# Performance work log

Hardware: AMD Instinct MI355X
Metric: run time of the kernel (lower is better)

Reference implementation:

```python
import jax, jax.numpy as jnp
import numpy as np

N, D, H, K, L, C = 65536, 512, 256, 16, 3, 64  # n_support, embed_dim, D//2, max_clusters, num_levels, n_classes
EPS = 1e-5


def setup_inputs() -> dict:
    key = jax.random.key(0)
    ks = jax.random.split(key, 18)
    s = 0.02
    inp = {
        "support_features": jax.random.normal(ks[0], (N, D), jnp.float32),
        "support_labels": jax.random.randint(ks[1], (N,), 0, C),
        # cluster heads (per level): Linear(D,H) -> ReLU -> Linear(H,K) -> Softmax
        "ch_w1": jax.random.normal(ks[2], (L, D, H), jnp.float32) * s,
        "ch_b1": jnp.zeros((L, H), jnp.float32),
        "ch_w2": jax.random.normal(ks[3], (L, H, K), jnp.float32) * s,
        "ch_b2": jnp.zeros((L, K), jnp.float32),
        # prototype refiners (per level): Linear(D,D) -> LayerNorm -> ReLU -> Linear(D,D)
        "ref_w1": jax.random.normal(ks[4], (L, D, D), jnp.float32) * s,
        "ref_b1": jnp.zeros((L, D), jnp.float32),
        "ln_g": jnp.ones((L, D), jnp.float32),
        "ln_b": jnp.zeros((L, D), jnp.float32),
        "ref_w2": jax.random.normal(ks[5], (L, D, D), jnp.float32) * s,
        "ref_b2": jnp.zeros((L, D), jnp.float32),
        # hierarchy combiner: Linear(L*D, D) -> ReLU -> Linear(D, D)
        "comb_w1": jax.random.normal(ks[6], (L * D, D), jnp.float32) * s,
        "comb_b1": jnp.zeros((D,), jnp.float32),
        "comb_w2": jax.random.normal(ks[7], (D, D), jnp.float32) * s,
        "comb_b2": jnp.zeros((D,), jnp.float32),
    }
    return inp


def _layernorm(x, g, b):
    m = x.mean(-1, keepdims=True)
    v = ((x - m) ** 2).mean(-1, keepdims=True)
    return (x - m) * jax.lax.rsqrt(v + EPS) * g + b


def reference(support_features, support_labels, ch_w1, ch_b1, ch_w2, ch_b2,
              ref_w1, ref_b1, ln_g, ln_b, ref_w2, ref_b2,
              comb_w1, comb_b1, comb_w2, comb_b2):
    current = support_features  # [N, D]; per-class offsets applied via label gather
    level_protos = []
    for l in range(L):
        # cluster head; softmax omitted since argmax is softmax-invariant
        logits = jax.nn.relu(current @ ch_w1[l] + ch_b1[l]) @ ch_w2[l] + ch_b2[l]  # [N, K]
        assign = jnp.argmax(logits, axis=-1)  # [N]
        seg = support_labels * K + assign  # combined (class, cluster) segment id
        sums = jax.ops.segment_sum(current, seg, num_segments=C * K)  # [C*K, D]
        cnt = jax.ops.segment_sum(jnp.ones((N,), current.dtype), seg, num_segments=C * K)
        means = sums / jnp.maximum(cnt, 1.0)[:, None]  # empty clusters -> 0, masked below
        h = means @ ref_w1[l] + ref_b1[l]
        h = jax.nn.relu(_layernorm(h, ln_g[l], ln_b[l]))
        refined = (h @ ref_w2[l] + ref_b2[l]).reshape(C, K, D)
        ne = (cnt.reshape(C, K) > 0).astype(current.dtype)  # non-empty cluster mask
        lp = (refined * ne[..., None]).sum(1) / ne.sum(1)[:, None]  # [C, D] mean over non-empty
        level_protos.append(lp)
        current = current + lp[support_labels]
    combined = jnp.concatenate(level_protos, axis=-1)  # [C, L*D]
    protos = jax.nn.relu(combined @ comb_w1 + comb_b1) @ comb_w2 + comb_b2  # [C, D]
    return protos
```

## Files before the change

kernel.cpp:

```cpp
#include <hip/hip_runtime.h>

#define NPTS 65536
#define DIM  512
#define HID  256
#define KCL  16
#define NLVL 3
#define NCLS 64
#define NSEG (NCLS*KCL)
#define EPSF 1e-5f

typedef __bf16 bf16_t;
typedef bf16_t bf16x4 __attribute__((ext_vector_type(4)));
typedef bf16_t bf16x8 __attribute__((ext_vector_type(8)));
typedef float  f32x4  __attribute__((ext_vector_type(4)));

#define LDA 40
#define LDH2 68

__global__ __launch_bounds__(256) void wsplit_kernel(
    const float* __restrict__ w1, bf16_t* __restrict__ hiT, bf16_t* __restrict__ loT)
{
  int gid = blockIdx.x * 256 + threadIdx.x;
  int n = gid >> 9, k = gid & 511;
  int l = n >> 8, j = n & 255;
  float v = w1[l*DIM*HID + k*HID + j];
  bf16_t h = (bf16_t)v;
  hiT[gid] = h;
  loT[gid] = (bf16_t)(v - (float)h);
}

__global__ __launch_bounds__(256) void wsplit2_kernel(
    const float* __restrict__ w1, const float* __restrict__ w2,
    bf16_t* __restrict__ h1, bf16_t* __restrict__ l1,
    bf16_t* __restrict__ h2, bf16_t* __restrict__ l2)
{
  const int per = NLVL*DIM*DIM;
  int gid = blockIdx.x * 256 + threadIdx.x;
  const float* w = (gid < per) ? w1 : w2;
  bf16_t* hh = (gid < per) ? h1 : h2;
  bf16_t* ll = (gid < per) ? l1 : l2;
  int g2 = (gid < per) ? gid : gid - per;
  int n512 = g2 >> 9, k = g2 & 511;
  int l = n512 >> 9, n = n512 & 511;
  float v = w[(size_t)l*DIM*DIM + (size_t)k*DIM + n];
  bf16_t h = (bf16_t)v;
  hh[g2] = h;
  ll[g2] = (bf16_t)(v - (float)h);
}

__global__ __launch_bounds__(256) void wsplitW2_kernel(
    const float* __restrict__ w2, bf16_t* __restrict__ hiT, bf16_t* __restrict__ loT)
{
  int gid = blockIdx.x * 256 + threadIdx.x;
  int l = gid >> 12, rem = gid & 4095;
  int k2 = rem >> 8, k = rem & 255;
  float v = w2[(size_t)l*HID*KCL + k*KCL + k2];
  bf16_t h = (bf16_t)v;
  hiT[gid] = h;
  loT[gid] = (bf16_t)(v - (float)h);
}

__global__ __launch_bounds__(512, 4) void gemmassign_kernel(
    const float* __restrict__ feat,
    const bf16_t* __restrict__ BhiT, const bf16_t* __restrict__ BloT,
    const bf16_t* __restrict__ w2hT, const bf16_t* __restrict__ w2lT,
    const float* __restrict__ offsrc, int ldo,
    const int* __restrict__ labels,
    const float* __restrict__ pb2,
    int* __restrict__ asg, int* __restrict__ cnt)
{
  __shared__ __align__(16) unsigned char SMraw[2*128*LDH2*4];
  __shared__ int labs[128];
  bf16_t* SM  = (bf16_t*)SMraw;
  bf16_t* Ahi = SM;
  bf16_t* Alo = SM + 128*LDA;
  bf16_t* Bhi = SM + 256*LDA;
  bf16_t* Blo = SM + 512*LDA;

  const int t = threadIdx.x;
  const int row0 = blockIdx.x * 128;
  const int w = t >> 6, lane = t & 63;
  const int wm = w & 1, wn = w >> 1;
  const int fm = lane & 15, fq = lane >> 4;

  if (t < 128) labs[t] = labels[row0 + t];
  const float pv = pb2[fm];

  f32x4 acc[4][4];
  #pragma unroll
  for (int i = 0; i < 4; i++)
    #pragma unroll
    for (int j = 0; j < 4; j++)
      #pragma unroll
      for (int r = 0; r < 4; r++) acc[i][j][r] = 0.f;

  for (int kc = 0; kc < DIM; kc += 32) {
    __syncthreads();
    #pragma unroll
    for (int p = 0; p < 2; p++) {
      int idx = t + 512*p;
      int r = idx >> 3, c = idx & 7;
      float4 v = *(const float4*)&feat[(size_t)(row0 + r)*DIM + kc + c*4];
      bf16x4 hi, lo;
      hi[0] = (bf16_t)v.x; lo[0] = (bf16_t)(v.x - (float)hi[0]);
      hi[1] = (bf16_t)v.y; lo[1] = (bf16_t)(v.y - (float)hi[1]);
      hi[2] = (bf16_t)v.z; lo[2] = (bf16_t)(v.z - (float)hi[2]);
      hi[3] = (bf16_t)v.w; lo[3] = (bf16_t)(v.w - (float)hi[3]);
      *(bf16x4*)&Ahi[r*LDA + c*4] = hi;
      *(bf16x4*)&Alo[r*LDA + c*4] = lo;
    }
    #pragma unroll
    for (int p = 0; p < 2; p++) {
      int idx = t + 512*p;
      int n = idx >> 2, c = idx & 3;
      *(bf16x8*)&Bhi[n*LDA + c*8] = *(const bf16x8*)&BhiT[(size_t)n*DIM + kc + c*8];
      *(bf16x8*)&Blo[n*LDA + c*8] = *(const bf16x8*)&BloT[(size_t)n*DIM + kc + c*8];
    }
    __syncthreads();

    bf16x8 ah[4], al[4], bh[4], bl[4];
    #pragma unroll
    for (int mt = 0; mt < 4; mt++) {
      int rr = (wm*64 + mt*16 + fm)*LDA + fq*8;
      ah[mt] = *(bf16x8*)&Ahi[rr];
      al[mt] = *(bf16x8*)&Alo[rr];
    }
    #pragma unroll
    for (int nt = 0; nt < 4; nt++) {
      int rr = (wn*64 + nt*16 + fm)*LDA + fq*8;
      bh[nt] = *(bf16x8*)&Bhi[rr];
      bl[nt] = *(bf16x8*)&Blo[rr];
    }
    #pragma unroll
    for (int mt = 0; mt < 4; mt++)
      #pragma unroll
      for (int nt = 0; nt < 4; nt++) {
        acc[mt][nt] = __builtin_amdgcn_mfma_f32_16x16x32_bf16(ah[mt], bh[nt], acc[mt][nt], 0, 0, 0);
        acc[mt][nt] = __builtin_amdgcn_mfma_f32_16x16x32_bf16(ah[mt], bl[nt], acc[mt][nt], 0, 0, 0);
        acc[mt][nt] = __builtin_amdgcn_mfma_f32_16x16x32_bf16(al[mt], bh[nt], acc[mt][nt], 0, 0, 0);
      }
  }

  __syncthreads();
  float* hA = (float*)SMraw;
  float* hB = hA + 128*LDH2;

  auto writeQ = [&](int q, float* buf) {
    #pragma unroll
    for (int nt = 0; nt < 4; nt++) {
      int colq = nt*16 + fm;
      int colg = q*64 + colq;
      #pragma unroll
      for (int mt = 0; mt < 4; mt++)
        #pragma unroll
        for (int r = 0; r < 4; r++) {
          int row = wm*64 + mt*16 + fq*4 + r;
          buf[row*LDH2 + colq] =
              fmaxf(acc[mt][nt][r] + offsrc[(size_t)labs[row]*ldo + colg], 0.f);
        }
    }
  };

  f32x4 lg = {0.f, 0.f, 0.f, 0.f};

  if (wn == 0) writeQ(0, hA);
  __syncthreads();
  #pragma unroll
  for (int q = 0; q < 4; q++) {
    float* cur = (q & 1) ? hB : hA;
    float* nxt = (q & 1) ? hA : hB;
    if (q < 3 && wn == q + 1) writeQ(q + 1, nxt);

    #pragma unroll
    for (int s = 0; s < 2; s++) {
      int kb = s*32 + fq*8;
      f32x4 a0 = *(f32x4*)&cur[(w*16 + fm)*LDH2 + kb];
      f32x4 a1 = *(f32x4*)&cur[(w*16 + fm)*LDH2 + kb + 4];
      bf16x8 ahf, alf;
      #pragma unroll
      for (int j = 0; j < 4; j++) {
        bf16_t h0 = (bf16_t)a0[j]; ahf[j]   = h0; alf[j]   = (bf16_t)(a0[j] - (float)h0);
        bf16_t h1 = (bf16_t)a1[j]; ahf[4+j] = h1; alf[4+j] = (bf16_t)(a1[j] - (float)h1);
      }
      bf16x8 bhf = *(const bf16x8*)&w2hT[fm*HID + q*64 + kb];
      bf16x8 blf = *(const bf16x8*)&w2lT[fm*HID + q*64 + kb];
      lg = __builtin_amdgcn_mfma_f32_16x16x32_bf16(ahf, bhf, lg, 0, 0, 0);
      lg = __builtin_amdgcn_mfma_f32_16x16x32_bf16(ahf, blf, lg, 0, 0, 0);
      lg = __builtin_amdgcn_mfma_f32_16x16x32_bf16(alf, bhf, lg, 0, 0, 0);
    }
    if (q < 3) __syncthreads();
  }

  #pragma unroll
  for (int r = 0; r < 4; r++) {
    float v = lg[r] + pv;
    int idx = fm;
    #pragma unroll
    for (int ofs = 8; ofs > 0; ofs >>= 1) {
      float ov = __shfl_xor(v, ofs, 16);
      int   oi = __shfl_xor(idx, ofs, 16);
      if (ov > v || (ov == v && oi < idx)) { v = ov; idx = oi; }
    }
    if (fm == 0) {
      int rloc = w*16 + fq*4 + r;
      asg[row0 + rloc] = idx;
      atomicAdd(&cnt[labs[rloc]*KCL + idx], 1);
    }
  }
}

__global__ __launch_bounds__(256) void gemm64_kernel(
    const float* __restrict__ Asrc,
    const bf16_t* __restrict__ BhiT, const bf16_t* __restrict__ BloT,
    float* __restrict__ C, int mode,
    const int* __restrict__ cnt, const float* __restrict__ off,
    const float* __restrict__ b1, const float* __restrict__ g,
    const float* __restrict__ bb, float* __restrict__ mP)
{
  __shared__ __align__(16) bf16_t Ahi[64*LDA];
  __shared__ __align__(16) bf16_t Alo[64*LDA];
  __shared__ __align__(16) bf16_t Bhi[64*LDA];
  __shared__ __align__(16) bf16_t Blo[64*LDA];
  __shared__ float rm[64], rr_[64];

  const int t = threadIdx.x;
  const int row0 = blockIdx.x * 64, col0 = blockIdx.y * 64;
  const int w = t >> 6, lane = t & 63;
  const int wm = w & 1, wn = w >> 1;
  const int fm = lane & 15, fq = lane >> 4;

  if (t < 64) {
    if (mode == 1) {
      int n = cnt[row0 + t];
      rm[t] = (float)n;
      rr_[t] = 1.f / fmaxf((float)n, 1.f);
    } else {
      float s1 = mP[row0 + t], s2 = mP[NSEG + row0 + t];
      float m = s1 * (1.f/512.f);
      float var = s2 * (1.f/512.f) - m*m;
      rm[t] = m;
      rr_[t] = rsqrtf(var + EPSF);
    }
  }

  f32x4 acc[2][2];
  #pragma unroll
  for (int i = 0; i < 2; i++)
    #pragma unroll
    for (int j = 0; j < 2; j++)
      #pragma unroll
      for (int r = 0; r < 4; r++) acc[i][j][r] = 0.f;

  for (int kc = 0; kc < DIM; kc += 32) {
    __syncthreads();
    #pragma unroll
    for (int p = 0; p < 2; p++) {
      int idx = t + 256*p;
      int r = idx >> 3, c = idx & 7;
      float4 v = *(const float4*)&Asrc[(size_t)(row0 + r)*DIM + kc + c*4];
      if (mode == 1) {
        int cls = (row0 + r) >> 4;
        float4 o = *(const float4*)&off[(size_t)cls*DIM + kc + c*4];
        float n = rm[r], inv = rr_[r];
        v.x = (v.x + n*o.x) * inv; v.y = (v.y + n*o.y) * inv;
        v.z = (v.z + n*o.z) * inv; v.w = (v.w + n*o.w) * inv;
      } else {
        float4 B1 = *(const float4*)&b1[kc + c*4];
        float4 G4 = *(const float4*)&g[kc + c*4];
        float4 BB = *(const float4*)&bb[kc + c*4];
        float m = rm[r], rs = rr_[r];
        v.x = fmaxf((v.x + B1.x - m)*rs*G4.x + BB.x, 0.f);
        v.y = fmaxf((v.y + B1.y - m)*rs*G4.y + BB.y, 0.f);
        v.z = fmaxf((v.z + B1.z - m)*rs*G4.z + BB.z, 0.f);
        v.w = fmaxf((v.w + B1.w - m)*rs*G4.w + BB.w, 0.f);
      }
      bf16x4 hi, lo;
      hi[0] = (bf16_t)v.x; lo[0] = (bf16_t)(v.x - (float)hi[0]);
      hi[1] = (bf16_t)v.y; lo[1] = (bf16_t)(v.y - (float)hi[1]);
      hi[2] = (bf16_t)v.z; lo[2] = (bf16_t)(v.z - (float)hi[2]);
      hi[3] = (bf16_t)v.w; lo[3] = (bf16_t)(v.w - (float)hi[3]);
      *(bf16x4*)&Ahi[r*LDA + c*4] = hi;
      *(bf16x4*)&Alo[r*LDA + c*4] = lo;
    }
    {
      int n = t >> 2, kof = (t & 3)*8;
      *(bf16x8*)&Bhi[n*LDA + kof] = *(const bf16x8*)&BhiT[(size_t)(col0 + n)*DIM + kc + kof];
      *(bf16x8*)&Blo[n*LDA + kof] = *(const bf16x8*)&BloT[(size_t)(col0 + n)*DIM + kc + kof];
    }
    __syncthreads();

    bf16x8 ah[2], al[2], bh[2], bl[2];
    #pragma unroll
    for (int mt = 0; mt < 2; mt++) {
      int idx = (wm*32 + mt*16 + fm)*LDA + fq*8;
      ah[mt] = *(bf16x8*)&Ahi[idx];
      al[mt] = *(bf16x8*)&Alo[idx];
    }
    #pragma unroll
    for (int nt = 0; nt < 2; nt++) {
      int idx = (wn*32 + nt*16 + fm)*LDA + fq*8;
      bh[nt] = *(bf16x8*)&Bhi[idx];
      bl[nt] = *(bf16x8*)&Blo[idx];
    }
    #pragma unroll
    for (int mt = 0; mt < 2; mt++)
      #pragma unroll
      for (int nt = 0; nt < 2; nt++) {
        acc[mt][nt] = __builtin_amdgcn_mfma_f32_16x16x32_bf16(ah[mt], bh[nt], acc[mt][nt], 0, 0, 0);
        acc[mt][nt] = __builtin_amdgcn_mfma_f32_16x16x32_bf16(ah[mt], bl[nt], acc[mt][nt], 0, 0, 0);
        acc[mt][nt] = __builtin_amdgcn_mfma_f32_16x16x32_bf16(al[mt], bh[nt], acc[mt][nt], 0, 0, 0);
        acc[mt][nt] = __builtin_amdgcn_mfma_f32_16x16x32_bf16(al[mt], bl[nt], acc[mt][nt], 0, 0, 0);
      }
  }

  #pragma unroll
  for (int mt = 0; mt < 2; mt++)
    #pragma unroll
    for (int nt = 0; nt < 2; nt++) {
      int col = col0 + wn*32 + nt*16 + fm;
      int rowb = row0 + wm*32 + mt*16 + fq*4;
      #pragma unroll
      for (int r = 0; r < 4; r++)
        C[(size_t)(rowb + r)*DIM + col] = acc[mt][nt][r];
    }

  if (mode == 1) {
    float b1v[2];
    #pragma unroll
    for (int nt = 0; nt < 2; nt++) b1v[nt] = b1[col0 + wn*32 + nt*16 + fm];
    #pragma unroll
    for (int mt = 0; mt < 2; mt++)
      #pragma unroll
      for (int r = 0; r < 4; r++) {
        float c1 = 0.f, c2 = 0.f;
        #pragma unroll
        for (int nt = 0; nt < 2; nt++) {
          float v = acc[mt][nt][r] + b1v[nt];
          c1 += v; c2 += v*v;
        }
        #pragma unroll
        for (int ofs = 8; ofs > 0; ofs >>= 1) {
          c1 += __shfl_xor(c1, ofs, 16);
          c2 += __shfl_xor(c2, ofs, 16);
        }
        if (fm == 0) {
          int row = row0 + wm*32 + mt*16 + fq*4 + r;
          atomicAdd(&mP[row], c1);
          atomicAdd(&mP[NSEG + row], c2);
        }
      }
  }
}

__global__ __launch_bounds__(256) void protoOffgemm_kernel(
    const float* __restrict__ Y2, const float* __restrict__ b2,
    const int* __restrict__ cnt, float* __restrict__ off, float* __restrict__ lp_out,
    const float* __restrict__ w1next, const float* __restrict__ b1next,
    float* __restrict__ offW1b)
{
  __shared__ float offs[DIM];
  int c = blockIdx.x, t = threadIdx.x;
  int nes = 0;
  #pragma unroll
  for (int k = 0; k < KCL; k++) nes += (cnt[c*KCL + k] > 0);
  float inv = 1.f / (float)nes;
  #pragma unroll
  for (int h = 0; h < 2; h++) {
    int d = t + h*256;
    float s = 0.f;
    #pragma unroll
    for (int k = 0; k < KCL; k++)
      if (cnt[c*KCL + k] > 0) s += Y2[(size_t)(c*KCL + k)*DIM + d];
    float lp = s * inv + b2[d];
    lp_out[c*DIM + d] = lp;
    float on = off[c*DIM + d] + lp;
    off[c*DIM + d] = on;
    offs[d] = on;
  }
  if (w1next == nullptr) return;
  __syncthreads();
  float a0 = 0.f, a1 = 0.f, a2 = 0.f, a3 = 0.f;
  #pragma unroll 4
  for (int d = 0; d < DIM; d += 4) {
    a0 = fmaf(offs[d+0], w1next[(d+0)*HID + t], a0);
    a1 = fmaf(offs[d+1], w1next[(d+1)*HID + t], a1);
    a2 = fmaf(offs[d+2], w1next[(d+2)*HID + t], a2);
    a3 = fmaf(offs[d+3], w1next[(d+3)*HID + t], a3);
  }
  offW1b[c*HID + t] = ((a0 + a1) + (a2 + a3)) + b1next[t];
}

__global__ void scan_kernel(const int* __restrict__ cnt, int* __restrict__ seg_st,
                            int* __restrict__ cursor)
{
  int t = threadIdx.x;
  int4 v = *(const int4*)&cnt[t*4];
  int a0 = v.x, a1 = v.x + v.y, a2 = a1 + v.z, tot = a2 + v.w;
  int lane = t & 63, w = t >> 6;
  int sc = tot;
  #pragma unroll
  for (int ofs = 1; ofs < 64; ofs <<= 1) {
    int u = __shfl_up(sc, ofs);
    if (lane >= ofs) sc += u;
  }
  __shared__ int wt[4];
  if (lane == 63) wt[w] = sc;
  __syncthreads();
  int base = 0;
  #pragma unroll
  for (int i = 0; i < 4; i++) if (i < w) base += wt[i];
  int excl = base + sc - tot;
  seg_st[t*4 + 1] = excl + a0;
  seg_st[t*4 + 2] = excl + a1;
  seg_st[t*4 + 3] = excl + a2;
  seg_st[t*4 + 4] = excl + tot;
  if (t == 0) seg_st[0] = 0;
  int4 cur = {excl, excl + a0, excl + a1, excl + a2};
  *(int4*)&cursor[t*4] = cur;
}

__global__ __launch_bounds__(256) void scatter_kernel(
    const int* __restrict__ labels, const int* __restrict__ asg,
    int* __restrict__ cursor, int* __restrict__ rowlist, int* __restrict__ seglist)
{
  int i = blockIdx.x * 256 + threadIdx.x;
  int seg = labels[i]*KCL + asg[i];
  int pos = atomicAdd(&cursor[seg], 1);
  rowlist[pos] = i;
  seglist[pos] = seg;
}

__global__ __launch_bounds__(256) void means3_kernel(
    const float* __restrict__ feat, const int* __restrict__ rowlist,
    const int* __restrict__ seglist, float* __restrict__ sums)
{
  __shared__ int rows[64];
  __shared__ int segs[65];
  int t = threadIdx.x;
  int i0 = blockIdx.x * 64;
  int col = blockIdx.y * 256 + t;
  if (t < 64) { rows[t] = rowlist[i0 + t]; segs[t] = seglist[i0 + t]; }
  if (t == 64) segs[64] = -1;
  __syncthreads();
  float acc = 0.f;
  for (int base = 0; base < 64; base += 16) {
    float v[16];
    #pragma unroll
    for (int j = 0; j < 16; j++)
      v[j] = feat[(size_t)rows[base + j]*DIM + col];
    #pragma unroll
    for (int j = 0; j < 16; j++) {
      acc += v[j];
      if (segs[base + j] != segs[base + j + 1]) {
        atomicAdd(&sums[(size_t)segs[base + j]*DIM + col], acc);
        acc = 0.f;
      }
    }
  }
}

__global__ __launch_bounds__(256) void fgemm1_kernel(
    const float* __restrict__ lp_all, const float* __restrict__ cw1,
    float* __restrict__ Hacc)
{
  __shared__ float As[64*132];
  __shared__ float Ws[128*64];
  int t = threadIdx.x;
  int nc = blockIdx.x * 64, kc = blockIdx.y * 128;

  #pragma unroll
  for (int p = 0; p < 8; p++) {
    int i = t + 256*p;
    int m = i >> 5, k0 = (i & 31) << 2;
    int k = kc + k0;
    int l = k >> 9, d = k & 511;
    *(float4*)&As[m*132 + k0] = *(const float4*)&lp_all[(size_t)(l*NCLS + m)*DIM + d];
  }
  #pragma unroll
  for (int p = 0; p < 8; p++) {
    int i = t + 256*p;
    int k = i >> 4, n0 = (i & 15) << 2;
    *(float4*)&Ws[k*64 + n0] = *(const float4*)&cw1[(size_t)(kc + k)*DIM + nc + n0];
  }
  __syncthreads();

  int tn = (t & 15) * 4, tmg = (t >> 4) * 4;
  float acc[4][4];
  #pragma unroll
  for (int i = 0; i < 4; i++)
    #pragma unroll
    for (int j = 0; j < 4; j++) acc[i][j] = 0.f;

  for (int k = 0; k < 128; k += 4) {
    float4 a[4], w[4];
    #pragma unroll
    for (int i = 0; i < 4; i++) a[i] = *(float4*)&As[(tmg + i)*132 + k];
    #pragma unroll
    for (int j = 0; j < 4; j++) w[j] = *(float4*)&Ws[(k + j)*64 + tn];
    #pragma unroll
    for (int kk = 0; kk < 4; kk++) {
      float wv[4] = {w[kk].x, w[kk].y, w[kk].z, w[kk].w};
      float av[4] = {a[0][kk], a[1][kk], a[2][kk], a[3][kk]};
      #pragma unroll
      for (int i = 0; i < 4; i++)
        #pragma unroll
        for (int j = 0; j < 4; j++)
          acc[i][j] = fmaf(av[i], wv[j], acc[i][j]);
    }
  }
  #pragma unroll
  for (int i = 0; i < 4; i++)
    #pragma unroll
    for (int j = 0; j < 4; j++)
      atomicAdd(&Hacc[(size_t)(tmg + i)*DIM + nc + tn + j], acc[i][j]);
}

__global__ __launch_bounds__(256) void fgemm2_kernel(
    const float* __restrict__ Hacc, const float* __restrict__ cb1,
    const float* __restrict__ cw2, float* __restrict__ Oacc)
{
  __shared__ float As[64*132];
  __shared__ float Ws[128*64];
  int t = threadIdx.x;
  int nc = blockIdx.x * 64, kc = blockIdx.y * 128;

  #pragma unroll
  for (int p = 0; p < 8; p++) {
    int i = t + 256*p;
    int m = i >> 5, k0 = (i & 31) << 2;
    float4 v = *(const float4*)&Hacc[(size_t)m*DIM + kc + k0];
    float4 b = *(const float4*)&cb1[kc + k0];
    v.x = fmaxf(v.x + b.x, 0.f); v.y = fmaxf(v.y + b.y, 0.f);
    v.z = fmaxf(v.z + b.z, 0.f); v.w = fmaxf(v.w + b.w, 0.f);
    *(float4*)&As[m*132 + k0] = v;
  }
  #pragma unroll
  for (int p = 0; p < 8; p++) {
    int i = t + 256*p;
    int k = i >> 4, n0 = (i & 15) << 2;
    *(float4*)&Ws[k*64 + n0] = *(const float4*)&cw2[(size_t)(kc + k)*DIM + nc + n0];
  }
  __syncthreads();

  int tn = (t & 15) * 4, tmg = (t >> 4) * 4;
  float acc[4][4];
  #pragma unroll
  for (int i = 0; i < 4; i++)
    #pragma unroll
    for (int j = 0; j < 4; j++) acc[i][j] = 0.f;

  for (int k = 0; k < 128; k += 4) {
    float4 a[4], w[4];
    #pragma unroll
    for (int i = 0; i < 4; i++) a[i] = *(float4*)&As[(tmg + i)*132 + k];
    #pragma unroll
    for (int j = 0; j < 4; j++) w[j] = *(float4*)&Ws[(k + j)*64 + tn];
    #pragma unroll
    for (int kk = 0; kk < 4; kk++) {
      float wv[4] = {w[kk].x, w[kk].y, w[kk].z, w[kk].w};
      float av[4] = {a[0][kk], a[1][kk], a[2][kk], a[3][kk]};
      #pragma unroll
      for (int i = 0; i < 4; i++)
        #pragma unroll
        for (int j = 0; j < 4; j++)
          acc[i][j] = fmaf(av[i], wv[j], acc[i][j]);
    }
  }
  #pragma unroll
  for (int i = 0; i < 4; i++)
    #pragma unroll
    for (int j = 0; j < 4; j++)
      atomicAdd(&Oacc[(size_t)(tmg + i)*DIM + nc + tn + j], acc[i][j]);
}

__global__ __launch_bounds__(256) void fbias_kernel(
    const float* __restrict__ Oacc, const float* __restrict__ cb2,
    float* __restrict__ out)
{
  int gi = blockIdx.x * 256 + threadIdx.x;
  out[gi] = Oacc[gi] + cb2[gi & 511];
}

extern "C" void kernel_launch(void* const* d_in, const int* in_sizes, int n_in,
                              void* d_out, int out_size, void* d_ws, size_t ws_size,
                              hipStream_t stream) {
  const float* feat   = (const float*)d_in[0];
  const int*   labels = (const int*)d_in[1];
  const float* ch_w1  = (const float*)d_in[2];
  const float* ch_b1  = (const float*)d_in[3];
  const float* ch_w2  = (const float*)d_in[4];
  const float* ch_b2  = (const float*)d_in[5];
  const float* ref_w1 = (const float*)d_in[6];
  const float* ref_b1 = (const float*)d_in[7];
  const float* ln_g   = (const float*)d_in[8];
  const float* ln_b   = (const float*)d_in[9];
  const float* ref_w2 = (const float*)d_in[10];
  const float* ref_b2 = (const float*)d_in[11];
  const float* cw1    = (const float*)d_in[12];
  const float* cb1    = (const float*)d_in[13];
  const float* cw2    = (const float*)d_in[14];
  const float* cb2    = (const float*)d_in[15];
  float* out = (float*)d_out;

  float* wsf = (float*)d_ws;
  float* off    = wsf;
  float* lp_all = off + 32768;
  float* sums   = lp_all + 98304;
  int*   cnt_i  = (int*)(sums + 524288);
  float* mP     = (float*)(cnt_i + NSEG);
  float* offW1b = mP + 2*NSEG;
  float* Hacc   = offW1b + 16384;
  float* Oacc   = Hacc + 32768;
  float* Y1     = Oacc + 32768;
  float* Y2     = Y1 + 524288;

  bf16_t* whiT  = (bf16_t*)(Y2 + 524288);
  bf16_t* wloT  = whiT + (size_t)NLVL*HID*DIM;
  bf16_t* r1hiT = wloT + (size_t)NLVL*HID*DIM;
  bf16_t* r1loT = r1hiT + (size_t)NLVL*DIM*DIM;
  bf16_t* r2hiT = r1loT + (size_t)NLVL*DIM*DIM;
  bf16_t* r2loT = r2hiT + (size_t)NLVL*DIM*DIM;
  bf16_t* w2hT  = r2loT + (size_t)NLVL*DIM*DIM;
  bf16_t* w2lT  = w2hT + (size_t)NLVL*KCL*HID;
  int* asg     = (int*)(w2lT + (size_t)NLVL*KCL*HID);
  int* rowlist = asg + NPTS;
  int* seglist = rowlist + NPTS;
  int* seg_st  = seglist + NPTS;
  int* cursor  = seg_st + 1040;

  hipMemsetAsync(off, 0, NCLS*DIM*sizeof(float), stream);

  wsplit_kernel<<<NLVL*HID*DIM/256, 256, 0, stream>>>(ch_w1, whiT, wloT);
  wsplit2_kernel<<<2*NLVL*DIM*DIM/256, 256, 0, stream>>>(
      ref_w1, ref_w2, r1hiT, r1loT, r2hiT, r2loT);
  wsplitW2_kernel<<<NLVL*KCL*HID/256, 256, 0, stream>>>(ch_w2, w2hT, w2lT);

  for (int l = 0; l < NLVL; l++) {
    hipMemsetAsync(sums, 0, (NSEG*DIM + NSEG + 2*NSEG)*sizeof(float), stream);

    const float* offsrc = (l == 0) ? ch_b1 : offW1b;
    int ldo = (l == 0) ? 0 : HID;

    gemmassign_kernel<<<NPTS/128, 512, 0, stream>>>(
        feat, whiT + (size_t)l*HID*DIM, wloT + (size_t)l*HID*DIM,
        w2hT + (size_t)l*KCL*HID, w2lT + (size_t)l*KCL*HID,
        offsrc, ldo, labels,
        ch_b2 + (size_t)l*KCL,
        asg, cnt_i);

    scan_kernel<<<1, 256, 0, stream>>>(cnt_i, seg_st, cursor);

    scatter_kernel<<<NPTS/256, 256, 0, stream>>>(labels, asg, cursor, rowlist, seglist);

    means3_kernel<<<dim3(NPTS/64, DIM/256), 256, 0, stream>>>(
        feat, rowlist, seglist, sums);

    gemm64_kernel<<<dim3(NSEG/64, DIM/64), 256, 0, stream>>>(
        sums, r1hiT + (size_t)l*DIM*DIM, r1loT + (size_t)l*DIM*DIM, Y1, 1,
        cnt_i, off, ref_b1 + (size_t)l*DIM, nullptr, nullptr, mP);

    gemm64_kernel<<<dim3(NSEG/64, DIM/64), 256, 0, stream>>>(
        Y1, r2hiT + (size_t)l*DIM*DIM, r2loT + (size_t)l*DIM*DIM, Y2, 2,
        nullptr, nullptr, ref_b1 + (size_t)l*DIM,
        ln_g + (size_t)l*DIM, ln_b + (size_t)l*DIM, mP);

    protoOffgemm_kernel<<<NCLS, 256, 0, stream>>>(
        Y2, ref_b2 + (size_t)l*DIM, cnt_i, off, lp_all + (size_t)l*NCLS*DIM,
        (l < NLVL-1) ? (ch_w1 + (size_t)(l+1)*DIM*HID) : nullptr,
        (l < NLVL-1) ? (ch_b1 + (size_t)(l+1)*HID) : nullptr,
        offW1b);
  }

  hipMemsetAsync(Hacc, 0, 2*NCLS*DIM*sizeof(float), stream);
  fgemm1_kernel<<<dim3(DIM/64, NLVL*DIM/128), 256, 0, stream>>>(lp_all, cw1, Hacc);
  fgemm2_kernel<<<dim3(DIM/64, DIM/128), 256, 0, stream>>>(Hacc, cb1, cw2, Oacc);
  fbias_kernel<<<NCLS*DIM/256, 256, 0, stream>>>(Oacc, cb2, out);
}
```

Baseline: 812.5 us.

## Split-K the second refiner GEMM with atomics and shrink gemmassign LDS to single buffer

The second refiner GEMM (mode 2) is split along K into two halves over blockIdx.z, and the partial results are accumulated into Y2 with atomicAdd. This doubles the block count for a small 1024x512 GEMM. Y2 is moved next to the zeroed region so the per-level memset clears it. Separately, gemmassign drops its double-buffered hidden-activation staging for a single buffer with an extra barrier per quarter. This reduces LDS use, which may allow more resident blocks, but serializes the writer and reader quarters.

New measurement: 783.7 us. 1.04x faster.

```diff
diff --git a/kernel.cpp b/kernel.cpp
--- a/kernel.cpp
+++ b/kernel.cpp
@@ -69,7 +69,7 @@
     const float* __restrict__ pb2,
     int* __restrict__ asg, int* __restrict__ cnt)
 {
-  __shared__ __align__(16) unsigned char SMraw[2*128*LDH2*4];
+  __shared__ __align__(16) unsigned char SMraw[768*LDA*2];
   __shared__ int labs[128];
   bf16_t* SM  = (bf16_t*)SMraw;
   bf16_t* Ahi = SM;
@@ -142,40 +142,35 @@
   }
 
   __syncthreads();
-  float* hA = (float*)SMraw;
-  float* hB = hA + 128*LDH2;
-
-  auto writeQ = [&](int q, float* buf) {
-    #pragma unroll
-    for (int nt = 0; nt < 4; nt++) {
-      int colq = nt*16 + fm;
-      int colg = q*64 + colq;
-      #pragma unroll
-      for (int mt = 0; mt < 4; mt++)
+  float* hS = (float*)SMraw;
+
+  f32x4 lg = {0.f, 0.f, 0.f, 0.f};
+
+  #pragma unroll
+  for (int q = 0; q < 4; q++) {
+    if (wn == q) {
+      #pragma unroll
+      for (int nt = 0; nt < 4; nt++) {
+        int colq = nt*16 + fm;
+        int colg = q*64 + colq;
         #pragma unroll
-        for (int r = 0; r < 4; r++) {
-          int row = wm*64 + mt*16 + fq*4 + r;
-          buf[row*LDH2 + colq] =
-              fmaxf(acc[mt][nt][r] + offsrc[(size_t)labs[row]*ldo + colg], 0.f);
-        }
-    }
-  };
-
-  f32x4 lg = {0.f, 0.f, 0.f, 0.f};
-
-  if (wn == 0) writeQ(0, hA);
-  __syncthreads();
-  #pragma unroll
-  for (int q = 0; q < 4; q++) {
-    float* cur = (q & 1) ? hB : hA;
-    float* nxt = (q & 1) ? hA : hB;
-    if (q < 3 && wn == q + 1) writeQ(q + 1, nxt);
+        for (int mt = 0; mt < 4; mt++)
+          #pragma unroll
+          for (int r = 0; r < 4; r++) {
+            int row = wm*64 + mt*16 + fq*4 + r;
+            float hv = fmaxf(acc[mt][nt][r] +
+                             offsrc[(size_t)labs[row]*ldo + colg], 0.f);
+            hS[row*LDH2 + colq] = hv;
+          }
+      }
+    }
+    __syncthreads();
 
     #pragma unroll
     for (int s = 0; s < 2; s++) {
       int kb = s*32 + fq*8;
-      f32x4 a0 = *(f32x4*)&cur[(w*16 + fm)*LDH2 + kb];
-      f32x4 a1 = *(f32x4*)&cur[(w*16 + fm)*LDH2 + kb + 4];
+      f32x4 a0 = *(f32x4*)&hS[(w*16 + fm)*LDH2 + kb];
+      f32x4 a1 = *(f32x4*)&hS[(w*16 + fm)*LDH2 + kb + 4];
       bf16x8 ahf, alf;
       #pragma unroll
       for (int j = 0; j < 4; j++) {
@@ -188,7 +183,7 @@
       lg = __builtin_amdgcn_mfma_f32_16x16x32_bf16(ahf, blf, lg, 0, 0, 0);
       lg = __builtin_amdgcn_mfma_f32_16x16x32_bf16(alf, bhf, lg, 0, 0, 0);
     }
-    if (q < 3) __syncthreads();
+    __syncthreads();
   }
 
   #pragma unroll
@@ -251,7 +246,10 @@
       #pragma unroll
       for (int r = 0; r < 4; r++) acc[i][j][r] = 0.f;
 
-  for (int kc = 0; kc < DIM; kc += 32) {
+  const int kstart = (mode == 2) ? blockIdx.z * 256 : 0;
+  const int kend   = (mode == 2) ? kstart + 256 : DIM;
+
+  for (int kc = kstart; kc < kend; kc += 32) {
     __syncthreads();
     #pragma unroll
     for (int p = 0; p < 2; p++) {
@@ -320,8 +318,12 @@
       int col = col0 + wn*32 + nt*16 + fm;
       int rowb = row0 + wm*32 + mt*16 + fq*4;
       #pragma unroll
-      for (int r = 0; r < 4; r++)
-        C[(size_t)(rowb + r)*DIM + col] = acc[mt][nt][r];
+      for (int r = 0; r < 4; r++) {
+        if (mode == 2)
+          atomicAdd(&C[(size_t)(rowb + r)*DIM + col], acc[mt][nt][r]);
+        else
+          C[(size_t)(rowb + r)*DIM + col] = acc[mt][nt][r];
+      }
     }
 
   if (mode == 1) {
@@ -608,13 +610,13 @@
   float* sums   = lp_all + 98304;
   int*   cnt_i  = (int*)(sums + 524288);
   float* mP     = (float*)(cnt_i + NSEG);
-  float* offW1b = mP + 2*NSEG;
+  float* Y2     = mP + 2*NSEG;
+  float* offW1b = Y2 + 524288;
   float* Hacc   = offW1b + 16384;
   float* Oacc   = Hacc + 32768;
   float* Y1     = Oacc + 32768;
-  float* Y2     = Y1 + 524288;
-
-  bf16_t* whiT  = (bf16_t*)(Y2 + 524288);
+
+  bf16_t* whiT  = (bf16_t*)(Y1 + 524288);
   bf16_t* wloT  = whiT + (size_t)NLVL*HID*DIM;
   bf16_t* r1hiT = wloT + (size_t)NLVL*HID*DIM;
   bf16_t* r1loT = r1hiT + (size_t)NLVL*DIM*DIM;
@@ -636,7 +638,7 @@
   wsplitW2_kernel<<<NLVL*KCL*HID/256, 256, 0, stream>>>(ch_w2, w2hT, w2lT);
 
   for (int l = 0; l < NLVL; l++) {
-    hipMemsetAsync(sums, 0, (NSEG*DIM + NSEG + 2*NSEG)*sizeof(float), stream);
+    hipMemsetAsync(sums, 0, (524288 + NSEG + 2*NSEG + 524288)*sizeof(float), stream);
 
     const float* offsrc = (l == 0) ? ch_b1 : offW1b;
     int ldo = (l == 0) ? 0 : HID;
@@ -655,11 +657,11 @@
     means3_kernel<<<dim3(NPTS/64, DIM/256), 256, 0, stream>>>(
         feat, rowlist, seglist, sums);
 
-    gemm64_kernel<<<dim3(NSEG/64, DIM/64), 256, 0, stream>>>(
+    gemm64_kernel<<<dim3(NSEG/64, DIM/64, 1), 256, 0, stream>>>(
         sums, r1hiT + (size_t)l*DIM*DIM, r1loT + (size_t)l*DIM*DIM, Y1, 1,
         cnt_i, off, ref_b1 + (size_t)l*DIM, nullptr, nullptr, mP);
 
-    gemm64_kernel<<<dim3(NSEG/64, DIM/64), 256, 0, stream>>>(
+    gemm64_kernel<<<dim3(NSEG/64, DIM/64, 2), 256, 0, stream>>>(
         Y1, r2hiT + (size_t)l*DIM*DIM, r2loT + (size_t)l*DIM*DIM, Y2, 2,
         nullptr, nullptr, ref_b1 + (size_t)l*DIM,
         ln_g + (size_t)l*DIM, ln_b + (size_t)l*DIM, mP);
```
